# Kernel optimization log

Measured on AMD Instinct MI355X. Metric: run time of the kernel, lower is better.

The kernel has to match this reference:

```python
import jax, jax.numpy as jnp
import numpy as np

ALPHA = 1.702
LIMIT = 7.0

def swiglu(h):
    # interleaved gating: even cols -> glu, odd cols -> linear
    x_glu = jnp.minimum(h[..., ::2], LIMIT)
    x_lin = jnp.clip(h[..., 1::2], -LIMIT, LIMIT)
    return x_glu * jax.nn.sigmoid(ALPHA * x_glu) * (x_lin + 1.0)

def setup_inputs() -> dict:
    E, T, D = 8, 2048, 2048
    key = jax.random.key(0)
    k1, k2, k3, k4, k5 = jax.random.split(key, 5)
    std = 0.02
    return {
        "x": jax.random.normal(k1, (E, T, D), dtype=jnp.float32),
        "mlp1_weight": jax.random.normal(k2, (E, D, 2 * D), dtype=jnp.float32) * std,
        "mlp1_bias": jax.random.normal(k3, (E, 2 * D), dtype=jnp.float32) * std,
        "mlp2_weight": jax.random.normal(k4, (E, D, D), dtype=jnp.float32) * std,
        "mlp2_bias": jax.random.normal(k5, (E, D), dtype=jnp.float32) * std,
    }

def reference(x, mlp1_weight, mlp1_bias, mlp2_weight, mlp2_bias):
    # per-expert batched MLP1 -> SwiGLU -> MLP2 (dense/balanced grouping)
    h = jnp.einsum('etd,edf->etf', x, mlp1_weight) + mlp1_bias[:, None, :]
    h = swiglu(h)
    out = jnp.einsum('etf,efd->etd', h, mlp2_weight) + mlp2_bias[:, None, :]
    return out
```

## Files before the change

kernel.cpp:

```cpp
#include <hip/hip_runtime.h>
#include <stdint.h>

typedef float f32x4 __attribute__((ext_vector_type(4)));
typedef short bf16x8 __attribute__((ext_vector_type(8)));

#define BM 128
#define BN 128
#define BK 32
#define LDA 40

__device__ __forceinline__ uint32_t pack_bf16(float a, float b) {
  uint32_t ua = __builtin_bit_cast(uint32_t, a);
  uint32_t ub = __builtin_bit_cast(uint32_t, b);
  ua += 0x8000u;
  ub += 0x8000u;
  return (ua >> 16) | (ub & 0xffff0000u);
}

template<bool A_BF16, bool SWIGLU>
__global__ __launch_bounds__(256)
void gemm_fused(const void* __restrict__ Aall,
                const float* __restrict__ Ball,
                const float* __restrict__ biasall,
                void* __restrict__ Outall,
                int M, int N, int K,
                long sA, long sB, long sBias, long sOut)
{
  __shared__ __align__(16) unsigned short As[BM * LDA];
  __shared__ __align__(16) unsigned short Bs[BN * LDA];

  const int e    = blockIdx.z;
  const int m0   = blockIdx.y * BM;
  const int n0   = blockIdx.x * BN;
  const int tid  = threadIdx.x;
  const int lane = tid & 63;
  const int q    = lane >> 4;
  const int c    = lane & 15;
  const int wave = tid >> 6;
  const int wm   = (wave >> 1) * 64;
  const int wn   = (wave & 1) * 64;

  const int ar = tid >> 1;
  const int ah = (tid & 1) * 16;
  const int bkg = (tid >> 5) * 4;
  const int bng = tid & 31;

  const float* Bbase = Ball + e * sB + (long)bkg * N + (n0 + bng);

  const float*          A32 = nullptr;
  const unsigned short* A16 = nullptr;
  if (A_BF16) A16 = (const unsigned short*)Aall + e * sA + (long)(m0 + ar) * K + ah;
  else        A32 = (const float*)Aall          + e * sA + (long)(m0 + ar) * K + ah;

  f32x4 acc[4][4];
#pragma unroll
  for (int i = 0; i < 4; i++)
#pragma unroll
    for (int j = 0; j < 4; j++)
      acc[i][j] = (f32x4){0.f, 0.f, 0.f, 0.f};

  for (int k0 = 0; k0 < K; k0 += BK) {
    __syncthreads();

    uint32_t ad[8];
    if (A_BF16) {
      const uint4* p = (const uint4*)(A16 + k0);
      uint4 u0 = p[0], u1 = p[1];
      ad[0] = u0.x; ad[1] = u0.y; ad[2] = u0.z; ad[3] = u0.w;
      ad[4] = u1.x; ad[5] = u1.y; ad[6] = u1.z; ad[7] = u1.w;
    } else {
      const float4* p = (const float4*)(A32 + k0);
      float4 f0 = p[0], f1 = p[1], f2 = p[2], f3 = p[3];
      ad[0] = pack_bf16(f0.x, f0.y); ad[1] = pack_bf16(f0.z, f0.w);
      ad[2] = pack_bf16(f1.x, f1.y); ad[3] = pack_bf16(f1.z, f1.w);
      ad[4] = pack_bf16(f2.x, f2.y); ad[5] = pack_bf16(f2.z, f2.w);
      ad[6] = pack_bf16(f3.x, f3.y); ad[7] = pack_bf16(f3.z, f3.w);
    }
    {
      uint4* dstA = (uint4*)&As[ar * LDA + ah];
      dstA[0] = make_uint4(ad[0], ad[1], ad[2], ad[3]);
      dstA[1] = make_uint4(ad[4], ad[5], ad[6], ad[7]);
    }

    {
      const float* Bp = Bbase + (long)k0 * N;
#pragma unroll
      for (int jj = 0; jj < 4; jj++) {
        float v0 = Bp[(long)0 * N + 32 * jj];
        float v1 = Bp[(long)1 * N + 32 * jj];
        float v2 = Bp[(long)2 * N + 32 * jj];
        float v3 = Bp[(long)3 * N + 32 * jj];
        uint2 w;
        w.x = pack_bf16(v0, v1);
        w.y = pack_bf16(v2, v3);
        *(uint2*)&Bs[(bng + 32 * jj) * LDA + bkg] = w;
      }
    }

    __syncthreads();

    bf16x8 af[4], bfr[4];
#pragma unroll
    for (int i = 0; i < 4; i++)
      af[i] = *(const bf16x8*)&As[(wm + i * 16 + c) * LDA + q * 8];
#pragma unroll
    for (int j = 0; j < 4; j++)
      bfr[j] = *(const bf16x8*)&Bs[(wn + j * 16 + c) * LDA + q * 8];
#pragma unroll
    for (int i = 0; i < 4; i++)
#pragma unroll
      for (int j = 0; j < 4; j++)
        acc[i][j] = __builtin_amdgcn_mfma_f32_16x16x32_bf16(af[i], bfr[j], acc[i][j], 0, 0, 0);
  }

  if (SWIGLU) {
    unsigned short* H = (unsigned short*)Outall + e * sOut;
    const int ldh = N >> 1;
#pragma unroll
    for (int j = 0; j < 4; j++) {
      const int f = n0 + wn + j * 16 + c;
      const float bias = biasall[e * sBias + f];
#pragma unroll
      for (int i = 0; i < 4; i++) {
        const int rb = m0 + wm + i * 16 + q * 4;
#pragma unroll
        for (int r = 0; r < 4; r++) {
          float v = acc[i][j][r] + bias;
          float p = __shfl_xor(v, 1);
          float xg = (f & 1) ? p : v;
          float xl = (f & 1) ? v : p;
          xg = fminf(xg, 7.f);
          xl = fminf(fmaxf(xl, -7.f), 7.f);
          float sig = 1.f / (1.f + __expf(-1.702f * xg));
          float res = xg * sig * (xl + 1.f);
          if ((f & 1) == 0) {
            uint32_t ub = __builtin_bit_cast(uint32_t, res) + 0x8000u;
            H[(long)(rb + r) * ldh + (f >> 1)] = (unsigned short)(ub >> 16);
          }
        }
      }
    }
  } else {
    float* O = (float*)Outall + e * sOut;
#pragma unroll
    for (int j = 0; j < 4; j++) {
      const int col = n0 + wn + j * 16 + c;
      const float bias = biasall[e * sBias + col];
#pragma unroll
      for (int i = 0; i < 4; i++) {
        const int rb = m0 + wm + i * 16 + q * 4;
#pragma unroll
        for (int r = 0; r < 4; r++)
          O[(long)(rb + r) * N + col] = acc[i][j][r] + bias;
      }
    }
  }
}

extern "C" void kernel_launch(void* const* d_in, const int* in_sizes, int n_in,
                              void* d_out, int out_size, void* d_ws, size_t ws_size,
                              hipStream_t stream) {
  const float* x  = (const float*)d_in[0];
  const float* w1 = (const float*)d_in[1];
  const float* b1 = (const float*)d_in[2];
  const float* w2 = (const float*)d_in[3];
  const float* b2 = (const float*)d_in[4];
  float* out = (float*)d_out;
  unsigned short* h = (unsigned short*)d_ws;

  const int E = 8, T = 2048, D = 2048;
  dim3 blk(256);

  dim3 g1((2 * D) / BN, T / BM, E);
  gemm_fused<false, true><<<g1, blk, 0, stream>>>(
      x, w1, b1, h,
      T, 2 * D, D,
      (long)T * D, (long)D * 2 * D, (long)2 * D, (long)T * D);

  dim3 g2(D / BN, T / BM, E);
  gemm_fused<true, false><<<g2, blk, 0, stream>>>(
      h, w2, b2, out,
      T, D, D,
      (long)T * D, (long)D * D, (long)D, (long)T * D);
}
```

Measured before the change: 1.285 ms.

## Pre-convert inputs to bf16 and stream tiles into LDS via global_load_lds

Adds pre-pass kernels that convert x to bf16 and transpose-convert both weight matrices into K-contiguous bf16 layouts, using workspace and the output buffer as scratch. The GEMMs then load bf16 tiles directly into LDS with global_load_lds, with no in-loop conversion, strided fp32 B reads or register staging. This removes per-tile conversion work and halves the bytes the GEMM loop reads from memory, at the cost of extra conversion passes. It also drops the LDS row padding, which risks bank conflicts on fragment reads. The original path is kept as a fallback when the workspace is too small.

```diff
diff --git a/kernel.cpp b/kernel.cpp
--- a/kernel.cpp
+++ b/kernel.cpp
@@ -8,6 +8,15 @@
 #define BN 128
 #define BK 32
 #define LDA 40
+
+#if defined(__has_builtin)
+#  if __has_builtin(__builtin_amdgcn_global_load_lds)
+#    define HAVE_GLLDS 1
+#  endif
+#endif
+#ifndef HAVE_GLLDS
+#  define HAVE_GLLDS 0
+#endif
 
 __device__ __forceinline__ uint32_t pack_bf16(float a, float b) {
   uint32_t ua = __builtin_bit_cast(uint32_t, a);
@@ -17,40 +26,88 @@
   return (ua >> 16) | (ub & 0xffff0000u);
 }
 
-template<bool A_BF16, bool SWIGLU>
+#if HAVE_GLLDS
+__device__ __forceinline__ void gload_lds16(const void* g, void* l) {
+  __builtin_amdgcn_global_load_lds(
+      (__attribute__((address_space(1))) void*)(uintptr_t)g,
+      (__attribute__((address_space(3))) void*)(uint32_t)(uintptr_t)l,
+      16, 0, 0);
+}
+#endif
+
+
 __global__ __launch_bounds__(256)
-void gemm_fused(const void* __restrict__ Aall,
-                const float* __restrict__ Ball,
-                const float* __restrict__ biasall,
-                void* __restrict__ Outall,
-                int M, int N, int K,
-                long sA, long sB, long sBias, long sOut)
+void cvt_f32_bf16(const float* __restrict__ src, unsigned short* __restrict__ dst, long n8) {
+  long i = (long)blockIdx.x * blockDim.x + threadIdx.x;
+  const long stride = (long)gridDim.x * blockDim.x;
+  for (; i < n8; i += stride) {
+    const float4* p = (const float4*)(src + i * 8);
+    float4 a = p[0], b = p[1];
+    uint4 o;
+    o.x = pack_bf16(a.x, a.y); o.y = pack_bf16(a.z, a.w);
+    o.z = pack_bf16(b.x, b.y); o.w = pack_bf16(b.z, b.w);
+    *(uint4*)(dst + i * 8) = o;
+  }
+}
+
+__global__ __launch_bounds__(256)
+void tcvt(const float* __restrict__ src, unsigned short* __restrict__ dst,
+          int K, int N, long sS, long sD) {
+  __shared__ float tile[64][33];
+  const int e = blockIdx.z;
+  const float* S = src + (long)e * sS;
+  unsigned short* Dp = dst + (long)e * sD;
+  const int k0 = blockIdx.y * 64;
+  const int n0 = blockIdx.x * 32;
+  const int tx = threadIdx.x & 31;
+  const int ty = threadIdx.x >> 5;
+#pragma unroll
+  for (int i = 0; i < 64; i += 8)
+    tile[ty + i][tx] = S[(long)(k0 + ty + i) * N + (n0 + tx)];
+  __syncthreads();
+#pragma unroll
+  for (int ii = 0; ii < 4; ii++) {
+    const int n = ty + 8 * ii;
+    const uint32_t w = pack_bf16(tile[2 * tx][n], tile[2 * tx + 1][n]);
+    *(uint32_t*)&Dp[(long)(n0 + n) * K + k0 + 2 * tx] = w;
+  }
+}
+
+template<bool SWIGLU>
+__global__ __launch_bounds__(256)
+void gemm_bf16(const unsigned short* __restrict__ A,
+               const unsigned short* __restrict__ B,
+               const float* __restrict__ biasall,
+               void* __restrict__ Outall,
+               int M, int N, int K,
+               long sA, long sB, long sBias, long sOut)
 {
-  __shared__ __align__(16) unsigned short As[BM * LDA];
-  __shared__ __align__(16) unsigned short Bs[BN * LDA];
+  __shared__ __align__(16) unsigned short As[BM * BK];
+  __shared__ __align__(16) unsigned short Bs[BN * BK];
 
   const int e    = blockIdx.z;
   const int m0   = blockIdx.y * BM;
   const int n0   = blockIdx.x * BN;
   const int tid  = threadIdx.x;
   const int lane = tid & 63;
+  const int wave = tid >> 6;
   const int q    = lane >> 4;
   const int c    = lane & 15;
-  const int wave = tid >> 6;
   const int wm   = (wave >> 1) * 64;
   const int wn   = (wave & 1) * 64;
 
-  const int ar = tid >> 1;
-  const int ah = (tid & 1) * 16;
-  const int bkg = (tid >> 5) * 4;
-  const int bng = tid & 31;
-
-  const float* Bbase = Ball + e * sB + (long)bkg * N + (n0 + bng);
-
-  const float*          A32 = nullptr;
-  const unsigned short* A16 = nullptr;
-  if (A_BF16) A16 = (const unsigned short*)Aall + e * sA + (long)(m0 + ar) * K + ah;
-  else        A32 = (const float*)Aall          + e * sA + (long)(m0 + ar) * K + ah;
+  const int stRow = wave * 16 + (lane >> 2);
+  const int stK   = (lane & 3) * 8;
+  const unsigned short* gA = A + e * sA + (long)(m0 + stRow) * K + stK;
+  const unsigned short* gB = B + e * sB + (long)(n0 + stRow) * K + stK;
+  const long rowK64 = 64L * K;
+
+  char* lA = (char*)As + wave * 1024;
+  char* lB = (char*)Bs + wave * 1024;
+#if !HAVE_GLLDS
+  char* lAp = (char*)As + wave * 1024 + lane * 16;
+  char* lBp = (char*)Bs + wave * 1024 + lane * 16;
+#endif
 
   f32x4 acc[4][4];
 #pragma unroll
@@ -60,52 +117,31 @@
       acc[i][j] = (f32x4){0.f, 0.f, 0.f, 0.f};
 
   for (int k0 = 0; k0 < K; k0 += BK) {
+    if (k0) __syncthreads();
+#if HAVE_GLLDS
+    gload_lds16(gA + k0,          lA);
+    gload_lds16(gA + k0 + rowK64, lA + 4096);
+    gload_lds16(gB + k0,          lB);
+    gload_lds16(gB + k0 + rowK64, lB + 4096);
+#else
+    {
+      uint4 ra0 = *(const uint4*)(gA + k0);
+      uint4 ra1 = *(const uint4*)(gA + k0 + rowK64);
+      uint4 rb0 = *(const uint4*)(gB + k0);
+      uint4 rb1 = *(const uint4*)(gB + k0 + rowK64);
+      *(uint4*)lAp = ra0; *(uint4*)(lAp + 4096) = ra1;
+      *(uint4*)lBp = rb0; *(uint4*)(lBp + 4096) = rb1;
+    }
+#endif
     __syncthreads();
 
-    uint32_t ad[8];
-    if (A_BF16) {
-      const uint4* p = (const uint4*)(A16 + k0);
-      uint4 u0 = p[0], u1 = p[1];
-      ad[0] = u0.x; ad[1] = u0.y; ad[2] = u0.z; ad[3] = u0.w;
-      ad[4] = u1.x; ad[5] = u1.y; ad[6] = u1.z; ad[7] = u1.w;
-    } else {
-      const float4* p = (const float4*)(A32 + k0);
-      float4 f0 = p[0], f1 = p[1], f2 = p[2], f3 = p[3];
-      ad[0] = pack_bf16(f0.x, f0.y); ad[1] = pack_bf16(f0.z, f0.w);
-      ad[2] = pack_bf16(f1.x, f1.y); ad[3] = pack_bf16(f1.z, f1.w);
-      ad[4] = pack_bf16(f2.x, f2.y); ad[5] = pack_bf16(f2.z, f2.w);
-      ad[6] = pack_bf16(f3.x, f3.y); ad[7] = pack_bf16(f3.z, f3.w);
-    }
-    {
-      uint4* dstA = (uint4*)&As[ar * LDA + ah];
-      dstA[0] = make_uint4(ad[0], ad[1], ad[2], ad[3]);
-      dstA[1] = make_uint4(ad[4], ad[5], ad[6], ad[7]);
-    }
-
-    {
-      const float* Bp = Bbase + (long)k0 * N;
-#pragma unroll
-      for (int jj = 0; jj < 4; jj++) {
-        float v0 = Bp[(long)0 * N + 32 * jj];
-        float v1 = Bp[(long)1 * N + 32 * jj];
-        float v2 = Bp[(long)2 * N + 32 * jj];
-        float v3 = Bp[(long)3 * N + 32 * jj];
-        uint2 w;
-        w.x = pack_bf16(v0, v1);
-        w.y = pack_bf16(v2, v3);
-        *(uint2*)&Bs[(bng + 32 * jj) * LDA + bkg] = w;
-      }
-    }
-
-    __syncthreads();
-
     bf16x8 af[4], bfr[4];
 #pragma unroll
     for (int i = 0; i < 4; i++)
-      af[i] = *(const bf16x8*)&As[(wm + i * 16 + c) * LDA + q * 8];
+      af[i] = *(const bf16x8*)&As[(wm + i * 16 + c) * BK + q * 8];
 #pragma unroll
     for (int j = 0; j < 4; j++)
-      bfr[j] = *(const bf16x8*)&Bs[(wn + j * 16 + c) * LDA + q * 8];
+      bfr[j] = *(const bf16x8*)&Bs[(wn + j * 16 + c) * BK + q * 8];
 #pragma unroll
     for (int i = 0; i < 4; i++)
 #pragma unroll
@@ -157,6 +193,143 @@
   }
 }
 
+template<bool A_BF16, bool SWIGLU>
+__global__ __launch_bounds__(256)
+void gemm_fused(const void* __restrict__ Aall,
+                const float* __restrict__ Ball,
+                const float* __restrict__ biasall,
+                void* __restrict__ Outall,
+                int M, int N, int K,
+                long sA, long sB, long sBias, long sOut)
+{
+  __shared__ __align__(16) unsigned short As[BM * LDA];
+  __shared__ __align__(16) unsigned short Bs[BN * LDA];
+
+  const int e    = blockIdx.z;
+  const int m0   = blockIdx.y * BM;
+  const int n0   = blockIdx.x * BN;
+  const int tid  = threadIdx.x;
+  const int lane = tid & 63;
+  const int q    = lane >> 4;
+  const int c    = lane & 15;
+  const int wave = tid >> 6;
+  const int wm   = (wave >> 1) * 64;
+  const int wn   = (wave & 1) * 64;
+
+  const int ar = tid >> 1;
+  const int ah = (tid & 1) * 16;
+  const int bkg = (tid >> 5) * 4;
+  const int bng = tid & 31;
+
+  const float* Bbase = Ball + e * sB + (long)bkg * N + (n0 + bng);
+
+  const float*          A32 = nullptr;
+  const unsigned short* A16 = nullptr;
+  if (A_BF16) A16 = (const unsigned short*)Aall + e * sA + (long)(m0 + ar) * K + ah;
+  else        A32 = (const float*)Aall          + e * sA + (long)(m0 + ar) * K + ah;
+
+  f32x4 acc[4][4];
+#pragma unroll
+  for (int i = 0; i < 4; i++)
+#pragma unroll
+    for (int j = 0; j < 4; j++)
+      acc[i][j] = (f32x4){0.f, 0.f, 0.f, 0.f};
+
+  for (int k0 = 0; k0 < K; k0 += BK) {
+    __syncthreads();
+    uint32_t ad[8];
+    if (A_BF16) {
+      const uint4* p = (const uint4*)(A16 + k0);
+      uint4 u0 = p[0], u1 = p[1];
+      ad[0] = u0.x; ad[1] = u0.y; ad[2] = u0.z; ad[3] = u0.w;
+      ad[4] = u1.x; ad[5] = u1.y; ad[6] = u1.z; ad[7] = u1.w;
+    } else {
+      const float4* p = (const float4*)(A32 + k0);
+      float4 f0 = p[0], f1 = p[1], f2 = p[2], f3 = p[3];
+      ad[0] = pack_bf16(f0.x, f0.y); ad[1] = pack_bf16(f0.z, f0.w);
+      ad[2] = pack_bf16(f1.x, f1.y); ad[3] = pack_bf16(f1.z, f1.w);
+      ad[4] = pack_bf16(f2.x, f2.y); ad[5] = pack_bf16(f2.z, f2.w);
+      ad[6] = pack_bf16(f3.x, f3.y); ad[7] = pack_bf16(f3.z, f3.w);
+    }
+    {
+      uint4* dstA = (uint4*)&As[ar * LDA + ah];
+      dstA[0] = make_uint4(ad[0], ad[1], ad[2], ad[3]);
+      dstA[1] = make_uint4(ad[4], ad[5], ad[6], ad[7]);
+    }
+    {
+      const float* Bp = Bbase + (long)k0 * N;
+#pragma unroll
+      for (int jj = 0; jj < 4; jj++) {
+        float v0 = Bp[(long)0 * N + 32 * jj];
+        float v1 = Bp[(long)1 * N + 32 * jj];
+        float v2 = Bp[(long)2 * N + 32 * jj];
+        float v3 = Bp[(long)3 * N + 32 * jj];
+        uint2 w;
+        w.x = pack_bf16(v0, v1);
+        w.y = pack_bf16(v2, v3);
+        *(uint2*)&Bs[(bng + 32 * jj) * LDA + bkg] = w;
+      }
+    }
+    __syncthreads();
+
+    bf16x8 af[4], bfr[4];
+#pragma unroll
+    for (int i = 0; i < 4; i++)
+      af[i] = *(const bf16x8*)&As[(wm + i * 16 + c) * LDA + q * 8];
+#pragma unroll
+    for (int j = 0; j < 4; j++)
+      bfr[j] = *(const bf16x8*)&Bs[(wn + j * 16 + c) * LDA + q * 8];
+#pragma unroll
+    for (int i = 0; i < 4; i++)
+#pragma unroll
+      for (int j = 0; j < 4; j++)
+        acc[i][j] = __builtin_amdgcn_mfma_f32_16x16x32_bf16(af[i], bfr[j], acc[i][j], 0, 0, 0);
+  }
+
+  if (SWIGLU) {
+    unsigned short* H = (unsigned short*)Outall + e * sOut;
+    const int ldh = N >> 1;
+#pragma unroll
+    for (int j = 0; j < 4; j++) {
+      const int f = n0 + wn + j * 16 + c;
+      const float bias = biasall[e * sBias + f];
+#pragma unroll
+      for (int i = 0; i < 4; i++) {
+        const int rb = m0 + wm + i * 16 + q * 4;
+#pragma unroll
+        for (int r = 0; r < 4; r++) {
+          float v = acc[i][j][r] + bias;
+          float p = __shfl_xor(v, 1);
+          float xg = (f & 1) ? p : v;
+          float xl = (f & 1) ? v : p;
+          xg = fminf(xg, 7.f);
+          xl = fminf(fmaxf(xl, -7.f), 7.f);
+          float sig = 1.f / (1.f + __expf(-1.702f * xg));
+          float res = xg * sig * (xl + 1.f);
+          if ((f & 1) == 0) {
+            uint32_t ub = __builtin_bit_cast(uint32_t, res) + 0x8000u;
+            H[(long)(rb + r) * ldh + (f >> 1)] = (unsigned short)(ub >> 16);
+          }
+        }
+      }
+    }
+  } else {
+    float* O = (float*)Outall + e * sOut;
+#pragma unroll
+    for (int j = 0; j < 4; j++) {
+      const int col = n0 + wn + j * 16 + c;
+      const float bias = biasall[e * sBias + col];
+#pragma unroll
+      for (int i = 0; i < 4; i++) {
+        const int rb = m0 + wm + i * 16 + q * 4;
+#pragma unroll
+        for (int r = 0; r < 4; r++)
+          O[(long)(rb + r) * N + col] = acc[i][j][r] + bias;
+      }
+    }
+  }
+}
+
 extern "C" void kernel_launch(void* const* d_in, const int* in_sizes, int n_in,
                               void* d_out, int out_size, void* d_ws, size_t ws_size,
                               hipStream_t stream) {
@@ -166,20 +339,35 @@
   const float* w2 = (const float*)d_in[3];
   const float* b2 = (const float*)d_in[4];
   float* out = (float*)d_out;
-  unsigned short* h = (unsigned short*)d_ws;
 
   const int E = 8, T = 2048, D = 2048;
+  const size_t elems = (size_t)E * T * D;
+  const size_t need  = elems * 2 * 2;
   dim3 blk(256);
 
-  dim3 g1((2 * D) / BN, T / BM, E);
-  gemm_fused<false, true><<<g1, blk, 0, stream>>>(
-      x, w1, b1, h,
-      T, 2 * D, D,
-      (long)T * D, (long)D * 2 * D, (long)2 * D, (long)T * D);
-
-  dim3 g2(D / BN, T / BM, E);
-  gemm_fused<true, false><<<g2, blk, 0, stream>>>(
-      h, w2, b2, out,
-      T, D, D,
-      (long)T * D, (long)D * D, (long)D, (long)T * D);
-}
+  if (ws_size >= need) {
+    unsigned short* scratch = (unsigned short*)d_ws;
+    unsigned short* h       = scratch + elems;
+    unsigned short* w1t     = (unsigned short*)d_out;
+
+    cvt_f32_bf16<<<dim3(2048), blk, 0, stream>>>(x, scratch, (long)(elems / 8));
+    tcvt<<<dim3((2 * D) / 32, D / 64, E), blk, 0, stream>>>(
+        w1, w1t, D, 2 * D, (long)D * 2 * D, (long)D * 2 * D);
+    gemm_bf16<true><<<dim3((2 * D) / BN, T / BM, E), blk, 0, stream>>>(
+        scratch, w1t, b1, h, T, 2 * D, D,
+        (long)T * D, (long)2 * D * D, (long)2 * D, (long)T * D);
+    tcvt<<<dim3(D / 32, D / 64, E), blk, 0, stream>>>(
+        w2, scratch, D, D, (long)D * D, (long)D * D);
+    gemm_bf16<false><<<dim3(D / BN, T / BM, E), blk, 0, stream>>>(
+        h, scratch, b2, out, T, D, D,
+        (long)T * D, (long)D * D, (long)D, (long)T * D);
+  } else {
+    unsigned short* h = (unsigned short*)d_ws;
+    gemm_fused<false, true><<<dim3((2 * D) / BN, T / BM, E), blk, 0, stream>>>(
+        x, w1, b1, h, T, 2 * D, D,
+        (long)T * D, (long)D * 2 * D, (long)2 * D, (long)T * D);
+    gemm_fused<true, false><<<dim3(D / BN, T / BM, E), blk, 0, stream>>>(
+        h, w2, b2, out, T, D, D,
+        (long)T * D, (long)D * D, (long)D, (long)T * D);
+  }
+}
```

New measurement: 1.116 ms. -13.1%, faster.
